# Performance work log

Measured on AMD Instinct MI355X. Metric: run time of the kernel, lower is better.

Reference implementation:

```python
import jax, jax.numpy as jnp
import numpy as np

CUTOFF = 5.0
N_RBF = 20
N_NODES, N_EDGES, F = 50000, 200000, 128


def setup_inputs() -> dict:
    key = jax.random.key(0)
    ks = jax.random.split(key, 11)
    inp = {
        "s": jax.random.normal(ks[0], (N_NODES, F), jnp.float32),
        "v": jax.random.normal(ks[1], (N_NODES, 3, F), jnp.float32),
        "rel_pos": jax.random.normal(ks[2], (N_EDGES, 3), jnp.float32),
        "W1": jax.random.normal(ks[3], (F, F), jnp.float32) * 0.05,
        "b1": jnp.zeros((F,), jnp.float32),
        "W2": jax.random.normal(ks[4], (F, 3 * F), jnp.float32) * 0.05,
        "b2": jnp.zeros((3 * F,), jnp.float32),
        "Wr": jax.random.normal(ks[5], (N_RBF, 3 * F), jnp.float32) * 0.05,
        "br": jnp.zeros((3 * F,), jnp.float32),
        "src": jax.random.randint(ks[6], (N_EDGES,), 0, N_NODES),
        "dst": jax.random.randint(ks[7], (N_EDGES,), 0, N_NODES),
    }
    return inp


def reference(s, v, rel_pos, W1, b1, W2, b2, Wr, br, src, dst):
    n_nodes, f = s.shape
    # phi MLP on node scalar features (computed per node, then gathered per edge)
    phi = jax.nn.silu(s @ W1 + b1) @ W2 + b2          # [N, 3F]
    phi_e = phi[src]                                   # [E, 3F]

    d = jnp.linalg.norm(rel_pos, axis=-1)              # [E]
    # sinc-style radial basis: sin(n*pi*d/cutoff)/d, n = 1..N_RBF
    n = jnp.arange(1, N_RBF + 1, dtype=d.dtype)
    rbf = jnp.sin(n * (jnp.pi / CUTOFF) * d[:, None]) / d[:, None]  # [E, 20]
    w_proj = rbf @ Wr + br                             # [E, 3F]
    # cosine cutoff gate
    fcut = 0.5 * (jnp.cos(jnp.pi * d / CUTOFF) + 1.0) * (d < CUTOFF)
    w = w_proj * fcut[:, None]                         # [E, 3F]

    split = w * phi_e                                  # hadamard gate, [E, 3F]
    s_v, s_s, s_r = split[:, :f], split[:, f:2 * f], split[:, 2 * f:]

    dirv = rel_pos / d[:, None]                        # r / ||r||, [E, 3]
    # vector message: gated neighbor vectors + gated directions
    dv = v[src] * s_v[:, None, :] + dirv[:, :, None] * s_r[:, None, :]  # [E,3,F]

    out_s = jax.ops.segment_sum(s_s, dst, num_segments=n_nodes)  # [N, F]
    out_v = jax.ops.segment_sum(dv, dst, num_segments=n_nodes)   # [N, 3, F]
    return out_v, out_s
```

## Files before the change

### kernel.cpp

```cpp
#include <hip/hip_runtime.h>
#include <math.h>

#define N_NODES_C 50000
#define N_EDGES_C 200000
#define FDIM 128
#define NRBF 20
#define CUT 5.0f
#define SC_BLK 196
#define GBLOCKS 12500
#define BATCH 32

typedef short  bf16x8 __attribute__((ext_vector_type(8)));
typedef float  f32x4  __attribute__((ext_vector_type(4)));
typedef unsigned int u32x3 __attribute__((ext_vector_type(3)));
typedef _Float16 f16x2 __attribute__((ext_vector_type(2)));

__device__ __forceinline__ unsigned short f32_to_bf16(float f) {
    unsigned u = __float_as_uint(f);
    unsigned r = (u + 0x7FFFu + ((u >> 16) & 1u)) >> 16;
    return (unsigned short)r;
}
__device__ __forceinline__ float bf16_to_f32(unsigned short h) {
    return __uint_as_float(((unsigned)h) << 16);
}
__device__ __forceinline__ unsigned short f16_bits(float x) {
    _Float16 h = (_Float16)x;
    unsigned short b;
    __builtin_memcpy(&b, &h, 2);
    return b;
}
__device__ __forceinline__ f16x2 u2h2(unsigned u) {
    f16x2 r;
    __builtin_memcpy(&r, &u, 4);
    return r;
}
__device__ __forceinline__ bf16x8 pack_bf16x8(float4 a, float4 b) {
    bf16x8 r;
    r[0] = (short)f32_to_bf16(a.x); r[1] = (short)f32_to_bf16(a.y);
    r[2] = (short)f32_to_bf16(a.z); r[3] = (short)f32_to_bf16(a.w);
    r[4] = (short)f32_to_bf16(b.x); r[5] = (short)f32_to_bf16(b.y);
    r[6] = (short)f32_to_bf16(b.z); r[7] = (short)f32_to_bf16(b.w);
    return r;
}

__global__ __launch_bounds__(256) void prep_all_kernel(
    const float* __restrict__ W1, const float* __restrict__ W2,
    const float* __restrict__ Wr, unsigned short* __restrict__ W1t,
    unsigned short* __restrict__ W2t, unsigned* __restrict__ wrh)
{
    int i = blockIdx.x * 256 + threadIdx.x;
    if (i < 128 * 128) {
        int n = i >> 7, k = i & 127;
        W1t[i] = f32_to_bf16(W1[k * 128 + n]);
    } else if (i < 128 * 128 + 384 * 128) {
        int j = i - 128 * 128;
        int n = j >> 7, k = j & 127;
        W2t[j] = f32_to_bf16(W2[k * 384 + n]);
    } else {
        int idx = i - (128 * 128 + 384 * 128);
        if (idx < 128 * 30) {
            int f  = idx / 30;
            int r  = idx % 30;
            int sec = r / 10, kp = r % 10;
            int col = sec * 128 + f;
            unsigned lo = f16_bits(Wr[(2 * kp)     * 384 + col]);
            unsigned hi = f16_bits(Wr[(2 * kp + 1) * 384 + col]);
            wrh[idx] = lo | (hi << 16);
        }
    }
}

__global__ __launch_bounds__(256) void mlp1w_kernel(
    const float* __restrict__ s, const unsigned short* __restrict__ W1t,
    const float* __restrict__ b1, unsigned short* __restrict__ h)
{
    __shared__ unsigned short w1lds[128 * 136];

    const int tid = threadIdx.x;
#pragma unroll
    for (int j = 0; j < 8; ++j) {
        int fi = tid + j * 256;
        int row  = fi >> 4;
        int colq = fi & 15;
        *(float4*)&w1lds[row * 136 + colq * 8] =
            *(const float4*)(W1t + (size_t)fi * 8);
    }
    __syncthreads();

    const int wv = tid >> 6, lane = tid & 63;
    const int m0 = blockIdx.x * 64 + wv * 16;
    const int lr = lane & 15, lg = lane >> 4;
    int arow = m0 + lr; if (arow >= N_NODES_C) arow = N_NODES_C - 1;

    f32x4 acc[8];
#pragma unroll
    for (int nt = 0; nt < 8; ++nt) acc[nt] = (f32x4){0.f, 0.f, 0.f, 0.f};

#pragma unroll
    for (int kt = 0; kt < 4; ++kt) {
        const int k0 = kt * 32 + lg * 8;
        const float4* ap = (const float4*)(s + (size_t)arow * 128 + k0);
        bf16x8 af = pack_bf16x8(ap[0], ap[1]);
#pragma unroll
        for (int nt = 0; nt < 8; ++nt) {
            bf16x8 bf = *(const bf16x8*)&w1lds[(nt * 16 + lr) * 136 + k0];
            acc[nt] = __builtin_amdgcn_mfma_f32_16x16x32_bf16(af, bf, acc[nt], 0, 0, 0);
        }
    }

    const int crow = m0 + lg * 4;
#pragma unroll
    for (int nt = 0; nt < 8; ++nt) {
        int col = nt * 16 + lr;
        float bb = b1[col];
#pragma unroll
        for (int r = 0; r < 4; ++r) {
            int m = crow + r;
            if (m < N_NODES_C) {
                float x = acc[nt][r] + bb;
                x = x / (1.f + __expf(-x));
                h[(size_t)m * 128 + col] = f32_to_bf16(x);
            }
        }
    }
}

__global__ __launch_bounds__(256) void mlp2pv_kernel(
    const unsigned short* __restrict__ h, const unsigned short* __restrict__ W2t,
    const float* __restrict__ b2, const float* __restrict__ v,
    unsigned short* __restrict__ pv)
{
    __shared__ unsigned short wlds[2][3 * 16 * 136];

    const int tid = threadIdx.x;
    const int wv = tid >> 6, lane = tid & 63;
    const int rg = wv & 1;
    const int hf = wv >> 1;
    const int m0 = blockIdx.x * 32 + rg * 16;
    const int lr = lane & 15, lg = lane >> 4;
    int arow = m0 + lr; if (arow >= N_NODES_C) arow = N_NODES_C - 1;

    bf16x8 af2[4];
#pragma unroll
    for (int kt = 0; kt < 4; ++kt)
        af2[kt] = *(const bf16x8*)(h + (size_t)arow * 128 + kt * 32 + lg * 8);

    const int crow = m0 + lg * 4;

    for (int t = 0; t < 4; ++t) {
        __syncthreads();
#pragma unroll
        for (int j = 0; j < 6; ++j) {
            int fi = tid + j * 256;
            int half = (fi >= 768) ? 1 : 0;
            int rem  = fi - half * 768;
            int c    = rem >> 8;
            int r2   = rem & 255;
            int row  = r2 >> 4;
            int colq = r2 & 15;
            int nt   = half * 4 + t;
            *(float4*)&wlds[half][(c * 16 + row) * 136 + colq * 8] =
                *(const float4*)(W2t +
                    ((size_t)(c * 128 + nt * 16 + row) * 128 + colq * 8));
        }
        __syncthreads();

        const unsigned short* W = wlds[hf];
        f32x4 a0 = (f32x4){0.f, 0.f, 0.f, 0.f};
        f32x4 a1 = (f32x4){0.f, 0.f, 0.f, 0.f};
        f32x4 a2 = (f32x4){0.f, 0.f, 0.f, 0.f};
#pragma unroll
        for (int kt = 0; kt < 4; ++kt) {
            const int k0 = kt * 32 + lg * 8;
            bf16x8 bf0 = *(const bf16x8*)&W[(      lr) * 136 + k0];
            bf16x8 bf1 = *(const bf16x8*)&W[(16 +  lr) * 136 + k0];
            bf16x8 bf2 = *(const bf16x8*)&W[(32 +  lr) * 136 + k0];
            a0 = __builtin_amdgcn_mfma_f32_16x16x32_bf16(af2[kt], bf0, a0, 0, 0, 0);
            a1 = __builtin_amdgcn_mfma_f32_16x16x32_bf16(af2[kt], bf1, a1, 0, 0, 0);
            a2 = __builtin_amdgcn_mfma_f32_16x16x32_bf16(af2[kt], bf2, a2, 0, 0, 0);
        }

        const int col = (hf * 4 + t) * 16 + lr;
        const float bb0 = b2[col], bb1 = b2[128 + col], bb2 = b2[256 + col];
#pragma unroll
        for (int r = 0; r < 4; ++r) {
            int m = crow + r;
            if (m < N_NODES_C) {
                const float* vr = v + (size_t)m * 384;
                unsigned p0 = f32_to_bf16(a0[r] + bb0);
                unsigned p1 = f32_to_bf16(a1[r] + bb1);
                unsigned p2 = f32_to_bf16(a2[r] + bb2);
                unsigned v0 = f32_to_bf16(vr[col]);
                unsigned v1 = f32_to_bf16(vr[128 + col]);
                unsigned v2 = f32_to_bf16(vr[256 + col]);
                u32x3 val;
                val.x = p0 | (p1 << 16);
                val.y = p2 | (v0 << 16);
                val.z = v1 | (v2 << 16);
                *(u32x3*)((char*)pv + (size_t)m * 1536 + (size_t)col * 12) = val;
            }
        }
    }
}

__global__ __launch_bounds__(256) void count_kernel(
    const int* __restrict__ dst, int* __restrict__ counts)
{
    int e = blockIdx.x * 256 + threadIdx.x;
    if (e < N_EDGES_C) atomicAdd(counts + dst[e], 1);
}

__global__ __launch_bounds__(256) void scan1_kernel(
    const int* __restrict__ counts, int* __restrict__ row_tmp,
    int* __restrict__ partial)
{
    __shared__ int sm[256];
    const int t = threadIdx.x;
    const int idx = blockIdx.x * 256 + t;
    int c = (idx < N_NODES_C) ? counts[idx] : 0;
    int x = c;
    sm[t] = x;
    __syncthreads();
#pragma unroll
    for (int off = 1; off < 256; off <<= 1) {
        int y = (t >= off) ? sm[t - off] : 0;
        __syncthreads();
        x += y;
        sm[t] = x;
        __syncthreads();
    }
    if (idx < N_NODES_C) row_tmp[idx] = x - c;
    if (t == 255) partial[blockIdx.x] = x;
}

__global__ __launch_bounds__(256) void scan2_kernel(
    const int* __restrict__ partial, int* __restrict__ poffs)
{
    __shared__ int sm[256];
    const int t = threadIdx.x;
    int c = (t < SC_BLK) ? partial[t] : 0;
    int x = c;
    sm[t] = x;
    __syncthreads();
#pragma unroll
    for (int off = 1; off < 256; off <<= 1) {
        int y = (t >= off) ? sm[t - off] : 0;
        __syncthreads();
        x += y;
        sm[t] = x;
        __syncthreads();
    }
    if (t < SC_BLK) poffs[t] = x - c;
}

__global__ __launch_bounds__(256) void scan3_kernel(
    const int* __restrict__ row_tmp, const int* __restrict__ poffs,
    int* __restrict__ row_ptr, int* __restrict__ row_fill)
{
    const int idx = blockIdx.x * 256 + threadIdx.x;
    if (idx < N_NODES_C) {
        int rp = row_tmp[idx] + poffs[blockIdx.x];
        row_ptr[idx]  = rp;
        row_fill[idx] = rp;
    }
    if (idx == 0) row_ptr[N_NODES_C] = N_EDGES_C;
}

__global__ __launch_bounds__(256) void fill_kernel(
    const float* __restrict__ rel_pos, const int* __restrict__ src,
    const int* __restrict__ dst, int* __restrict__ row_fill,
    float* __restrict__ e_meta)
{
    int e = blockIdx.x * 256 + threadIdx.x;
    if (e >= N_EDGES_C) return;

    int pos = atomicAdd(row_fill + dst[e], 1);

    float x = rel_pos[3 * e + 0];
    float y = rel_pos[3 * e + 1];
    float z = rel_pos[3 * e + 2];
    float d = sqrtf(x * x + y * y + z * z);
    float invd = 1.0f / d;

    float s1 = 0.f, c1 = 0.f, fcut = 0.f, amp = 0.f;
    if (d < CUT) {
        sincosf((3.14159265358979f / CUT) * d, &s1, &c1);
        fcut = 0.5f * (c1 + 1.0f);
        amp  = invd * fcut;
    }

    float rb[NRBF];
    float sk = s1, ck = c1;
#pragma unroll
    for (int k = 0; k < NRBF; ++k) {
        rb[k] = sk * amp;
        float sn = sk * c1 + ck * s1;
        ck = ck * c1 - sk * s1;
        sk = sn;
    }

    unsigned pk[10];
#pragma unroll
    for (int kp = 0; kp < 10; ++kp)
        pk[kp] = (unsigned)f16_bits(rb[2 * kp]) | ((unsigned)f16_bits(rb[2 * kp + 1]) << 16);

    float4* mp = (float4*)(e_meta + (size_t)pos * 16);
    mp[0] = make_float4(x * invd, y * invd, z * invd, fcut);
    mp[1] = make_float4(__uint_as_float(pk[0]), __uint_as_float(pk[1]),
                        __uint_as_float(pk[2]), __uint_as_float(pk[3]));
    mp[2] = make_float4(__uint_as_float(pk[4]), __uint_as_float(pk[5]),
                        __uint_as_float(pk[6]), __uint_as_float(pk[7]));
    mp[3] = make_float4(__uint_as_float(pk[8]), __uint_as_float(pk[9]),
                        __int_as_float(src[e]), 0.f);
}

#define COMPUTE_E(M_, U)                                                       \
    {                                                                          \
        const float4 m0 = *(const float4*)(M_);                                \
        const unsigned* mu_ = (const unsigned*)((M_) + 4);                     \
        float w0 = m0.w * br0, w1 = m0.w * br1, w2 = m0.w * br2;               \
        _Pragma("unroll")                                                      \
        for (int kp = 0; kp < 10; ++kp) {                                      \
            f16x2 rh = u2h2(mu_[kp]);                                          \
            w0 = __builtin_amdgcn_fdot2(rh, u2h2(wrp0[kp]), w0, false);        \
            w1 = __builtin_amdgcn_fdot2(rh, u2h2(wrp1[kp]), w1, false);        \
            w2 = __builtin_amdgcn_fdot2(rh, u2h2(wrp2[kp]), w2, false);        \
        }                                                                      \
        float P0 = bf16_to_f32((unsigned short)((U).x & 0xFFFFu));             \
        float P1 = bf16_to_f32((unsigned short)((U).x >> 16));                 \
        float P2 = bf16_to_f32((unsigned short)((U).y & 0xFFFFu));             \
        float V0 = bf16_to_f32((unsigned short)((U).y >> 16));                 \
        float V1 = bf16_to_f32((unsigned short)((U).z & 0xFFFFu));             \
        float V2 = bf16_to_f32((unsigned short)((U).z >> 16));                 \
        float sv = w0 * P0;                                                    \
        float ss = w1 * P1;                                                    \
        float sr = w2 * P2;                                                    \
        acc_s  += ss;                                                          \
        acc_v0 += V0 * sv + m0.x * sr;                                         \
        acc_v1 += V1 * sv + m0.y * sr;                                         \
        acc_v2 += V2 * sv + m0.z * sr;                                         \
    }

#define LOADPV(U, SI)                                                          \
    U = *(const u32x3*)((const char*)pv + (size_t)(SI) * 1536 + (size_t)f * 12);

#define STORE_NODE(N_, AS, A0, A1, A2)                                         \
    {                                                                          \
        out_s[(size_t)(N_) * 128 + f] = AS;                                    \
        out_v[(size_t)(N_) * 384 +       f] = A0;                              \
        out_v[(size_t)(N_) * 384 + 128 + f] = A1;                              \
        out_v[(size_t)(N_) * 384 + 256 + f] = A2;                              \
    }

#define BOUNDARY(GE)                                                           \
    if ((GE) + 1 == end_cur) {                                                 \
        STORE_NODE(cur, acc_s, acc_v0, acc_v1, acc_v2);                        \
        acc_s = acc_v0 = acc_v1 = acc_v2 = 0.f;                                \
        ++cur;                                                                 \
        while (cur < nhi) {                                                    \
            int ne_ = row_ptr[cur + 1];                                        \
            if (ne_ != (GE) + 1) { end_cur = ne_; break; }                     \
            STORE_NODE(cur, 0.f, 0.f, 0.f, 0.f);                               \
            ++cur;                                                             \
        }                                                                      \
    }

__global__ __launch_bounds__(128) void gather_packed_kernel(
    const unsigned short* __restrict__ pv, const unsigned* __restrict__ wrh,
    const float* __restrict__ br, const int* __restrict__ row_ptr,
    const float* __restrict__ e_meta,
    float* __restrict__ out_v, float* __restrict__ out_s)
{
    __shared__ float meta_lds[2][BATCH * 16];

    const int f = threadIdx.x;
    const int gid = blockIdx.x;
    const int chunk = (N_NODES_C + GBLOCKS - 1) / GBLOCKS;
    const int nlo = gid * chunk;
    if (nlo >= N_NODES_C) return;
    const int nhi = min(nlo + chunk, N_NODES_C);

    unsigned wrp0[10], wrp1[10], wrp2[10];
    {
        const unsigned* wp = wrh + (size_t)f * 30;
#pragma unroll
        for (int i = 0; i < 10; ++i) {
            wrp0[i] = wp[i];
            wrp1[i] = wp[10 + i];
            wrp2[i] = wp[20 + i];
        }
#pragma unroll
        for (int i = 0; i < 10; ++i)
            asm volatile("" : "+v"(wrp0[i]), "+v"(wrp1[i]), "+v"(wrp2[i]));
    }
    const float br0 = br[f], br1 = br[128 + f], br2 = br[256 + f];

    const int gbeg = row_ptr[nlo];
    const int gend = row_ptr[nhi];
    const int nedge = gend - gbeg;

    float acc_s = 0.f, acc_v0 = 0.f, acc_v1 = 0.f, acc_v2 = 0.f;

    int cur = nlo;
    while (cur < nhi && row_ptr[cur + 1] == gbeg) {
        STORE_NODE(cur, 0.f, 0.f, 0.f, 0.f);
        ++cur;
    }
    int end_cur = (cur < nhi) ? row_ptr[cur + 1] : gbeg;

    if (nedge > 0) {
        const float4* src0 = (const float4*)(e_meta + (size_t)gbeg * 16);
        ((float4*)meta_lds[0])[threadIdx.x] = src0[threadIdx.x];
    }
    __syncthreads();

    const int total_batches = (nedge + BATCH - 1) / BATCH;
    for (int b = 0; b < total_batches; ++b) {
        const int bstart = b * BATCH;
        const int bcount = min(BATCH, nedge - bstart);
        const bool have_next = (b + 1 < total_batches);

        float4 st;
        if (have_next)
            st = ((const float4*)(e_meta + (size_t)(gbeg + bstart + BATCH) * 16))[threadIdx.x];

        const float* Mb = meta_lds[b & 1];

        u32x3 uA, uB;
        {
            int si = ((const int*)Mb)[14];
            LOADPV(uA, si);
        }

        int t = 0;
        while (t < bcount) {
            if (t + 1 < bcount) {
                int si = ((const int*)(Mb + (t + 1) * 16))[14];
                LOADPV(uB, si);
            }
            COMPUTE_E(Mb + t * 16, uA);
            BOUNDARY(gbeg + bstart + t);
            ++t; if (t >= bcount) break;

            if (t + 1 < bcount) {
                int si = ((const int*)(Mb + (t + 1) * 16))[14];
                LOADPV(uA, si);
            }
            COMPUTE_E(Mb + t * 16, uB);
            BOUNDARY(gbeg + bstart + t);
            ++t;
        }

        if (have_next) ((float4*)meta_lds[(b + 1) & 1])[threadIdx.x] = st;
        __syncthreads();
    }
}

extern "C" void kernel_launch(void* const* d_in, const int* in_sizes, int n_in,
                              void* d_out, int out_size, void* d_ws, size_t ws_size,
                              hipStream_t stream)
{
    const float* s  = (const float*)d_in[0];
    const float* v  = (const float*)d_in[1];
    const float* rp = (const float*)d_in[2];
    const float* W1 = (const float*)d_in[3];
    const float* b1 = (const float*)d_in[4];
    const float* W2 = (const float*)d_in[5];
    const float* b2 = (const float*)d_in[6];
    const float* Wr = (const float*)d_in[7];
    const float* br = (const float*)d_in[8];
    const int* src  = (const int*)d_in[9];
    const int* dst  = (const int*)d_in[10];

    float* out   = (float*)d_out;
    float* out_v = out;
    float* out_s = out + (size_t)N_NODES_C * 3 * FDIM;

    char* ws = (char*)d_ws;
    float* e_meta = (float*)ws;                 ws += ((size_t)N_EDGES_C * 16 + 256) * sizeof(float);
    unsigned short* W1t = (unsigned short*)ws;  ws += (size_t)128 * 128 * sizeof(unsigned short);
    unsigned short* W2t = (unsigned short*)ws;  ws += (size_t)384 * 128 * sizeof(unsigned short);
    unsigned* wrh = (unsigned*)ws;              ws += (size_t)128 * 30 * sizeof(unsigned);
    int* counts   = (int*)ws;                   ws += (size_t)N_NODES_C * sizeof(int);
    int* row_ptr  = (int*)ws;                   ws += (size_t)(N_NODES_C + 4) * sizeof(int);
    int* row_fill = (int*)ws;                   ws += (size_t)N_NODES_C * sizeof(int);
    int* row_tmp  = (int*)ws;                   ws += (size_t)N_NODES_C * sizeof(int);
    int* partial  = (int*)ws;                   ws += (size_t)256 * sizeof(int);
    int* poffs    = (int*)ws;                   ws += (size_t)256 * sizeof(int);
    unsigned short* h = (unsigned short*)ws;    ws += (size_t)N_NODES_C * 128 * sizeof(unsigned short);
    unsigned short* pv = (unsigned short*)ws;

    hipMemsetAsync(counts, 0, (size_t)N_NODES_C * sizeof(int), stream);

    count_kernel<<<(N_EDGES_C + 255) / 256, 256, 0, stream>>>(dst, counts);
    scan1_kernel<<<SC_BLK, 256, 0, stream>>>(counts, row_tmp, partial);
    scan2_kernel<<<1, 256, 0, stream>>>(partial, poffs);
    scan3_kernel<<<SC_BLK, 256, 0, stream>>>(row_tmp, poffs, row_ptr, row_fill);
    fill_kernel<<<(N_EDGES_C + 255) / 256, 256, 0, stream>>>(rp, src, dst, row_fill, e_meta);

    prep_all_kernel<<<272, 256, 0, stream>>>(W1, W2, Wr, W1t, W2t, wrh);
    mlp1w_kernel<<<(N_NODES_C + 63) / 64, 256, 0, stream>>>(s, W1t, b1, h);
    mlp2pv_kernel<<<(N_NODES_C + 31) / 32, 256, 0, stream>>>(h, W2t, b2, v, pv);

    gather_packed_kernel<<<GBLOCKS, 128, 0, stream>>>(pv, wrh, br, row_ptr,
                                                      e_meta, out_v, out_s);
}
```

Measured before the change: 205.9 us.

## Split packed phi/v buffer into two 8-byte-aligned arrays and halve gather grid

The 12-byte interleaved phi+v record per node/feature becomes two padded 8-byte arrays: phi from the MLP2 kernel and a bf16 copy of v made by a new vpack kernel. The gather kernel then issues two aligned 8-byte loads per edge instead of one misaligned 12-byte load, and its grid drops from 12500 to 6250 blocks so each block covers more nodes. This costs an extra kernel launch, padding bytes, and two gather streams per edge instead of one.

New measurement: 205.2 us. No clear change (-0.3%).

```diff
diff --git a/kernel.cpp b/kernel.cpp
--- a/kernel.cpp
+++ b/kernel.cpp
@@ -7,12 +7,11 @@
 #define NRBF 20
 #define CUT 5.0f
 #define SC_BLK 196
-#define GBLOCKS 12500
+#define GBLOCKS 6250
 #define BATCH 32
 
 typedef short  bf16x8 __attribute__((ext_vector_type(8)));
 typedef float  f32x4  __attribute__((ext_vector_type(4)));
-typedef unsigned int u32x3 __attribute__((ext_vector_type(3)));
 typedef _Float16 f16x2 __attribute__((ext_vector_type(2)));
 
 __device__ __forceinline__ unsigned short f32_to_bf16(float f) {
@@ -70,6 +69,23 @@
     }
 }
 
+__global__ __launch_bounds__(256) void vpack_kernel(
+    const float* __restrict__ v, unsigned short* __restrict__ pvv)
+{
+    const int total = N_NODES_C * 128;
+    for (int idx = blockIdx.x * 256 + threadIdx.x; idx < total;
+         idx += gridDim.x * 256) {
+        int n = idx >> 7, f = idx & 127;
+        const float* vr = v + (size_t)n * 384;
+        ushort4 o;
+        o.x = f32_to_bf16(vr[f]);
+        o.y = f32_to_bf16(vr[128 + f]);
+        o.z = f32_to_bf16(vr[256 + f]);
+        o.w = 0;
+        *(ushort4*)(pvv + (size_t)idx * 4) = o;
+    }
+}
+
 __global__ __launch_bounds__(256) void mlp1w_kernel(
     const float* __restrict__ s, const unsigned short* __restrict__ W1t,
     const float* __restrict__ b1, unsigned short* __restrict__ h)
@@ -125,10 +141,9 @@
     }
 }
 
-__global__ __launch_bounds__(256) void mlp2pv_kernel(
+__global__ __launch_bounds__(256) void mlp2p_kernel(
     const unsigned short* __restrict__ h, const unsigned short* __restrict__ W2t,
-    const float* __restrict__ b2, const float* __restrict__ v,
-    unsigned short* __restrict__ pv)
+    const float* __restrict__ b2, unsigned short* __restrict__ pvp)
 {
     __shared__ unsigned short wlds[2][3 * 16 * 136];
 
@@ -186,18 +201,13 @@
         for (int r = 0; r < 4; ++r) {
             int m = crow + r;
             if (m < N_NODES_C) {
-                const float* vr = v + (size_t)m * 384;
                 unsigned p0 = f32_to_bf16(a0[r] + bb0);
                 unsigned p1 = f32_to_bf16(a1[r] + bb1);
                 unsigned p2 = f32_to_bf16(a2[r] + bb2);
-                unsigned v0 = f32_to_bf16(vr[col]);
-                unsigned v1 = f32_to_bf16(vr[128 + col]);
-                unsigned v2 = f32_to_bf16(vr[256 + col]);
-                u32x3 val;
+                uint2 val;
                 val.x = p0 | (p1 << 16);
-                val.y = p2 | (v0 << 16);
-                val.z = v1 | (v2 << 16);
-                *(u32x3*)((char*)pv + (size_t)m * 1536 + (size_t)col * 12) = val;
+                val.y = p2;
+                *(uint2*)(pvp + ((size_t)m * 128 + col) * 4) = val;
             }
         }
     }
@@ -314,7 +324,7 @@
                         __int_as_float(src[e]), 0.f);
 }
 
-#define COMPUTE_E(M_, U)                                                       \
+#define COMPUTE_E(M_, UP, UV)                                                  \
     {                                                                          \
         const float4 m0 = *(const float4*)(M_);                                \
         const unsigned* mu_ = (const unsigned*)((M_) + 4);                     \
@@ -326,12 +336,12 @@
             w1 = __builtin_amdgcn_fdot2(rh, u2h2(wrp1[kp]), w1, false);        \
             w2 = __builtin_amdgcn_fdot2(rh, u2h2(wrp2[kp]), w2, false);        \
         }                                                                      \
-        float P0 = bf16_to_f32((unsigned short)((U).x & 0xFFFFu));             \
-        float P1 = bf16_to_f32((unsigned short)((U).x >> 16));                 \
-        float P2 = bf16_to_f32((unsigned short)((U).y & 0xFFFFu));             \
-        float V0 = bf16_to_f32((unsigned short)((U).y >> 16));                 \
-        float V1 = bf16_to_f32((unsigned short)((U).z & 0xFFFFu));             \
-        float V2 = bf16_to_f32((unsigned short)((U).z >> 16));                 \
+        float P0 = bf16_to_f32((unsigned short)((UP).x & 0xFFFFu));            \
+        float P1 = bf16_to_f32((unsigned short)((UP).x >> 16));                \
+        float P2 = bf16_to_f32((unsigned short)((UP).y & 0xFFFFu));            \
+        float V0 = bf16_to_f32((unsigned short)((UV).x & 0xFFFFu));            \
+        float V1 = bf16_to_f32((unsigned short)((UV).x >> 16));                \
+        float V2 = bf16_to_f32((unsigned short)((UV).y & 0xFFFFu));            \
         float sv = w0 * P0;                                                    \
         float ss = w1 * P1;                                                    \
         float sr = w2 * P2;                                                    \
@@ -341,8 +351,9 @@
         acc_v2 += V2 * sv + m0.z * sr;                                         \
     }
 
-#define LOADPV(U, SI)                                                          \
-    U = *(const u32x3*)((const char*)pv + (size_t)(SI) * 1536 + (size_t)f * 12);
+#define LOADPV(UP, UV, SI)                                                     \
+    UP = *(const uint2*)(pvp + ((size_t)(SI) * 128 + f) * 4);                  \
+    UV = *(const uint2*)(pvv + ((size_t)(SI) * 128 + f) * 4);
 
 #define STORE_NODE(N_, AS, A0, A1, A2)                                         \
     {                                                                          \
@@ -366,9 +377,9 @@
     }
 
 __global__ __launch_bounds__(128) void gather_packed_kernel(
-    const unsigned short* __restrict__ pv, const unsigned* __restrict__ wrh,
-    const float* __restrict__ br, const int* __restrict__ row_ptr,
-    const float* __restrict__ e_meta,
+    const unsigned short* __restrict__ pvp, const unsigned short* __restrict__ pvv,
+    const unsigned* __restrict__ wrh, const float* __restrict__ br,
+    const int* __restrict__ row_ptr, const float* __restrict__ e_meta,
     float* __restrict__ out_v, float* __restrict__ out_s)
 {
     __shared__ float meta_lds[2][BATCH * 16];
@@ -426,27 +437,27 @@
 
         const float* Mb = meta_lds[b & 1];
 
-        u32x3 uA, uB;
+        uint2 upA, uvA, upB, uvB;
         {
             int si = ((const int*)Mb)[14];
-            LOADPV(uA, si);
+            LOADPV(upA, uvA, si);
         }
 
         int t = 0;
         while (t < bcount) {
             if (t + 1 < bcount) {
                 int si = ((const int*)(Mb + (t + 1) * 16))[14];
-                LOADPV(uB, si);
+                LOADPV(upB, uvB, si);
             }
-            COMPUTE_E(Mb + t * 16, uA);
+            COMPUTE_E(Mb + t * 16, upA, uvA);
             BOUNDARY(gbeg + bstart + t);
             ++t; if (t >= bcount) break;
 
             if (t + 1 < bcount) {
                 int si = ((const int*)(Mb + (t + 1) * 16))[14];
-                LOADPV(uA, si);
+                LOADPV(upA, uvA, si);
             }
-            COMPUTE_E(Mb + t * 16, uB);
+            COMPUTE_E(Mb + t * 16, upB, uvB);
             BOUNDARY(gbeg + bstart + t);
             ++t;
         }
@@ -488,7 +499,8 @@
     int* partial  = (int*)ws;                   ws += (size_t)256 * sizeof(int);
     int* poffs    = (int*)ws;                   ws += (size_t)256 * sizeof(int);
     unsigned short* h = (unsigned short*)ws;    ws += (size_t)N_NODES_C * 128 * sizeof(unsigned short);
-    unsigned short* pv = (unsigned short*)ws;
+    unsigned short* pvp = (unsigned short*)ws;  ws += (size_t)N_NODES_C * 128 * 4 * sizeof(unsigned short);
+    unsigned short* pvv = (unsigned short*)ws;
 
     hipMemsetAsync(counts, 0, (size_t)N_NODES_C * sizeof(int), stream);
 
@@ -499,9 +511,10 @@
     fill_kernel<<<(N_EDGES_C + 255) / 256, 256, 0, stream>>>(rp, src, dst, row_fill, e_meta);
 
     prep_all_kernel<<<272, 256, 0, stream>>>(W1, W2, Wr, W1t, W2t, wrh);
+    vpack_kernel<<<4096, 256, 0, stream>>>(v, pvv);
     mlp1w_kernel<<<(N_NODES_C + 63) / 64, 256, 0, stream>>>(s, W1t, b1, h);
-    mlp2pv_kernel<<<(N_NODES_C + 31) / 32, 256, 0, stream>>>(h, W2t, b2, v, pv);
-
-    gather_packed_kernel<<<GBLOCKS, 128, 0, stream>>>(pv, wrh, br, row_ptr,
+    mlp2p_kernel<<<(N_NODES_C + 31) / 32, 256, 0, stream>>>(h, W2t, b2, pvp);
+
+    gather_packed_kernel<<<GBLOCKS, 128, 0, stream>>>(pvp, pvv, wrh, br, row_ptr,
                                                       e_meta, out_v, out_s);
 }
```
